# Kernel optimization log

Measured on AMD Instinct MI355X. Metric: run time of the kernel, lower is better.

Reference implementation:

```python
import jax, jax.numpy as jnp
import numpy as np

B, TE, TD, DE, DD = 4, 256, 256, 512, 512


def setup_inputs() -> dict:
    key = jax.random.key(0)
    k1, k2, k3, k4, k5 = jax.random.split(key, 5)
    return {
        "encoder_outputs": jax.random.normal(k1, (B, TE, DE), dtype=jnp.float32),
        "decoder_outputs": jax.random.normal(k2, (B, TD, DD), dtype=jnp.float32),
        "U_a": jax.random.normal(k3, (DE, DE), dtype=jnp.float32) * 0.05,
        "W_a": jax.random.normal(k4, (DD, DE), dtype=jnp.float32) * 0.05,
        "V_a": jax.random.normal(k5, (DE,), dtype=jnp.float32) * 0.05,
    }


def reference(encoder_outputs, decoder_outputs, U_a, W_a, V_a):
    # U_a_dot_h: [B, Te, De] -- precomputed once, as in the original
    Uh = jnp.einsum("bec,cd->bed", encoder_outputs, U_a)
    # W_a_dot_s for all decoder steps at once (original loops over t): [B, Td, De]
    Ws = jnp.einsum("btc,cd->btd", decoder_outputs, W_a)
    # additive energies: tanh(Uh + Ws) . V_a -> [B, Td, Te]
    e = jnp.einsum("bted,d->bte", jnp.tanh(Uh[:, None, :, :] + Ws[:, :, None, :]), V_a)
    attn = jax.nn.softmax(e, axis=-1)  # softmax over encoder timesteps
    # context: weighted sum of encoder outputs -> [B, Td, De]
    context = jnp.einsum("bte,bec->btc", attn, encoder_outputs)
    return context, attn
```

## Files before the change

### kernel.cpp

```cpp
#include <hip/hip_runtime.h>

#define B_    4
#define TE_   256
#define TD_   256
#define DE_   512
#define K_    512

typedef __attribute__((ext_vector_type(8))) short bf16x8;
typedef __attribute__((ext_vector_type(4))) float f32x4;

#define C1F 2.8853900817779268f

__device__ __forceinline__ ushort f2bf(float x) {
  uint u = __float_as_uint(x);
  return (ushort)((u + 0x7fffu + ((u >> 16) & 1u)) >> 16);
}
__device__ __forceinline__ float bf2f(ushort h) {
  return __uint_as_float(((uint)h) << 16);
}
__device__ __forceinline__ float exp2_fast(float x) {
  float r;
  asm("v_exp_f32 %0, %1" : "=v"(r) : "v"(x));
  return r;
}

__global__ __launch_bounds__(256) void conv_hilo(
    const float* __restrict__ enc, const float* __restrict__ dec,
    ushort* __restrict__ ehi, ushort* __restrict__ elo,
    ushort* __restrict__ dhi, ushort* __restrict__ dlo) {
  const float* in = blockIdx.y ? dec : enc;
  ushort* hi = blockIdx.y ? dhi : ehi;
  ushort* lo = blockIdx.y ? dlo : elo;
  int i = (blockIdx.x * 256 + threadIdx.x) * 4;
  float4 v = *(const float4*)&in[i];
  ushort4 h, l;
  h.x = f2bf(v.x); l.x = f2bf(v.x - bf2f(h.x));
  h.y = f2bf(v.y); l.y = f2bf(v.y - bf2f(h.y));
  h.z = f2bf(v.z); l.z = f2bf(v.z - bf2f(h.z));
  h.w = f2bf(v.w); l.w = f2bf(v.w - bf2f(h.w));
  *(ushort4*)&hi[i] = h;
  *(ushort4*)&lo[i] = l;
}

__global__ __launch_bounds__(256) void conv_bt(
    const float* __restrict__ Ua, const float* __restrict__ Wa,
    ushort* __restrict__ uhi, ushort* __restrict__ ulo,
    ushort* __restrict__ whi, ushort* __restrict__ wlo) {
  const float* in = blockIdx.z ? Wa : Ua;
  ushort* thi = blockIdx.z ? whi : uhi;
  ushort* tlo = blockIdx.z ? wlo : ulo;
  __shared__ float tile[64][65];
  int k0 = blockIdx.y * 64, n0 = blockIdx.x * 64;
  int tid = threadIdx.x;
#pragma unroll
  for (int i = 0; i < 16; ++i) {
    int idx = tid + i * 256;
    int r = idx >> 6, c = idx & 63;
    tile[r][c] = in[(size_t)(k0 + r) * 512 + n0 + c];
  }
  __syncthreads();
#pragma unroll
  for (int i = 0; i < 16; ++i) {
    int idx = tid + i * 256;
    int rn = idx >> 6, ck = idx & 63;
    float x = tile[ck][rn] * C1F;
    ushort h = f2bf(x);
    size_t o = (size_t)(n0 + rn) * 512 + k0 + ck;
    thi[o] = h;
    tlo[o] = f2bf(x - bf2f(h));
  }
}

__global__ __launch_bounds__(256, 4) void gemm_mfma(
    const ushort* __restrict__ ehi, const ushort* __restrict__ elo,
    const ushort* __restrict__ dhi, const ushort* __restrict__ dlo,
    const ushort* __restrict__ uhi, const ushort* __restrict__ ulo,
    const ushort* __restrict__ whi, const ushort* __restrict__ wlo,
    float* __restrict__ EuT, float* __restrict__ Ew) {
  const ushort *Ahi, *Alo, *Bhi, *Blo;
  int tid = threadIdx.x, lane = tid & 63;
  int ti = blockIdx.x * 4 + (tid >> 6);
  int bm, bn;
  if (blockIdx.z == 0) {
    Ahi = uhi; Alo = ulo; Bhi = ehi; Blo = elo;
    bm = (ti >> 5) * 16; bn = (ti & 31) * 32;
  } else {
    Ahi = dhi; Alo = dlo; Bhi = whi; Blo = wlo;
    bm = (ti >> 4) * 16; bn = (ti & 15) * 32;
  }
  int frow = lane & 15, fk = (lane >> 4) * 8;
  size_t ao = (size_t)(bm + frow) * K_ + fk;
  size_t bo = (size_t)(bn + frow) * K_ + fk;
  const ushort* pah = Ahi + ao;
  const ushort* pal = Alo + ao;
  const ushort* pbh0 = Bhi + bo; const ushort* pbh1 = pbh0 + 16 * K_;
  const ushort* pbl0 = Blo + bo; const ushort* pbl1 = pbl0 + 16 * K_;
  f32x4 acc0 = {}, acc1 = {};
#pragma unroll 4
  for (int k0 = 0; k0 < K_; k0 += 32) {
    bf16x8 ah = *(const bf16x8*)&pah[k0];
    bf16x8 al = *(const bf16x8*)&pal[k0];
    bf16x8 bh0 = *(const bf16x8*)&pbh0[k0];
    bf16x8 bl0 = *(const bf16x8*)&pbl0[k0];
    bf16x8 bh1 = *(const bf16x8*)&pbh1[k0];
    bf16x8 bl1 = *(const bf16x8*)&pbl1[k0];
    acc0 = __builtin_amdgcn_mfma_f32_16x16x32_bf16(ah, bh0, acc0, 0, 0, 0);
    acc1 = __builtin_amdgcn_mfma_f32_16x16x32_bf16(ah, bh1, acc1, 0, 0, 0);
    acc0 = __builtin_amdgcn_mfma_f32_16x16x32_bf16(ah, bl0, acc0, 0, 0, 0);
    acc1 = __builtin_amdgcn_mfma_f32_16x16x32_bf16(ah, bl1, acc1, 0, 0, 0);
    acc0 = __builtin_amdgcn_mfma_f32_16x16x32_bf16(al, bh0, acc0, 0, 0, 0);
    acc1 = __builtin_amdgcn_mfma_f32_16x16x32_bf16(al, bh1, acc1, 0, 0, 0);
  }
  int m0 = bm + (lane >> 4) * 4;
#pragma unroll
  for (int j = 0; j < 2; ++j) {
    const f32x4& acc = j ? acc1 : acc0;
    int n0 = bn + j * 16 + (lane & 15);
    if (blockIdx.z == 0) {
      float* cb = EuT + (size_t)(n0 >> 8) * 131072 + (size_t)m0 * 256 + (n0 & 255);
#pragma unroll
      for (int r = 0; r < 4; ++r) cb[(size_t)r * 256] = exp2_fast(acc[r]);
    } else {
      float* cb = Ew + (size_t)m0 * 512 + n0;
#pragma unroll
      for (int r = 0; r < 4; ++r) cb[(size_t)r * 512] = exp2_fast(acc[r]);
    }
  }
}

__global__ __launch_bounds__(1024, 8) void fused_attn(
    const float* __restrict__ enc, const float* __restrict__ EuT,
    const float* __restrict__ Ew, const float* __restrict__ Va,
    float* __restrict__ out_ctx, float* __restrict__ out_attn) {
  int bt = blockIdx.x;
  int b  = bt >> 7;
  int t0 = (bt & 127) * 2;
  __shared__ float ew0_s[520], ew1_s[520], mv_s[520];
  __shared__ float part[32][260];
  __shared__ float att2[TE_ * 2];
  __shared__ float ctxp[2][2][512];
  __shared__ float redm[2][4], reds[2][4];
  int tid = threadIdx.x, lane = tid & 63, w = tid >> 6;

  if (tid < 512) {
    const float* ewr = Ew + (size_t)(b * TD_ + t0) * DE_;
    int pd = tid + (tid >> 6);
    ew0_s[pd] = ewr[tid];
    ew1_s[pd] = ewr[DE_ + tid];
    mv_s[pd]  = -2.0f * Va[tid];
  }
  __syncthreads();

  const float* up = EuT + (size_t)b * 131072 + (size_t)w * 32 * 256 + lane * 4;
  float a0[4] = {}, a1[4] = {};
#pragma unroll 4
  for (int row = 0; row < 32; ++row) {
    float4 u4 = *(const float4*)&up[row * 256];
    int d = w * 32 + row, pd = d + (d >> 6);
    float e0 = ew0_s[pd], e1 = ew1_s[pd], mv = mv_s[pd];
#pragma unroll
    for (int j = 0; j < 4; ++j) {
      float u = j == 0 ? u4.x : j == 1 ? u4.y : j == 2 ? u4.z : u4.w;
      a0[j] = fmaf(mv, __builtin_amdgcn_rcpf(fmaf(u, e0, 1.0f)), a0[j]);
      a1[j] = fmaf(mv, __builtin_amdgcn_rcpf(fmaf(u, e1, 1.0f)), a1[j]);
    }
  }
  *(float4*)&part[w * 2 + 0][lane * 4] = make_float4(a0[0], a0[1], a0[2], a0[3]);
  *(float4*)&part[w * 2 + 1][lane * 4] = make_float4(a1[0], a1[1], a1[2], a1[3]);
  __syncthreads();

  int t = tid >> 8, col = tid & 255;
  float x = 0.f, p = 0.f, m, s;
  if (tid < 512) {
#pragma unroll
    for (int ww = 0; ww < 16; ++ww) x += part[ww * 2 + t][col];
    m = x;
#pragma unroll
    for (int off = 32; off; off >>= 1) m = fmaxf(m, __shfl_xor(m, off));
    if (lane == 0) redm[t][w & 3] = m;
  }
  __syncthreads();
  if (tid < 512) {
    m = fmaxf(fmaxf(redm[t][0], redm[t][1]), fmaxf(redm[t][2], redm[t][3]));
    p = __expf(x - m);
    s = p;
#pragma unroll
    for (int off = 32; off; off >>= 1) s += __shfl_xor(s, off);
    if (lane == 0) reds[t][w & 3] = s;
  }
  __syncthreads();
  if (tid < 512) {
    s = reds[t][0] + reds[t][1] + reds[t][2] + reds[t][3];
    float a = p * __builtin_amdgcn_rcpf(s);
    att2[col * 2 + t] = a;
    out_attn[(size_t)(b * TD_ + t0 + t) * TE_ + col] = a;
  }
  __syncthreads();

  int d = tid & 511, half = tid >> 9;
  const float* enc_b = enc + (size_t)b * TE_ * DE_ + (size_t)half * 128 * DE_;
  float c0 = 0.f, c1 = 0.f;
#pragma unroll 4
  for (int ee = 0; ee < 128; ++ee) {
    float2 av = *(const float2*)&att2[(half * 128 + ee) * 2];
    float xv = enc_b[(size_t)ee * DE_ + d];
    c0 = fmaf(av.x, xv, c0);
    c1 = fmaf(av.y, xv, c1);
  }
  ctxp[half][0][d] = c0;
  ctxp[half][1][d] = c1;
  __syncthreads();
  int tt = tid >> 9, dd = tid & 511;
  out_ctx[(size_t)(b * TD_ + t0 + tt) * DE_ + dd] =
      ctxp[0][tt][dd] + ctxp[1][tt][dd];
}

extern "C" void kernel_launch(void* const* d_in, const int* in_sizes, int n_in,
                              void* d_out, int out_size, void* d_ws, size_t ws_size,
                              hipStream_t stream) {
  const float* enc = (const float*)d_in[0];
  const float* dec = (const float*)d_in[1];
  const float* Ua  = (const float*)d_in[2];
  const float* Wa  = (const float*)d_in[3];
  const float* Va  = (const float*)d_in[4];

  float* out_ctx  = (float*)d_out;
  float* out_attn = out_ctx + (size_t)B_ * TD_ * DE_;

  char* wsp = (char*)d_ws;
  float* EuT = (float*)wsp;             wsp += (size_t)B_ * DE_ * TE_ * 4;
  float* Ewm = (float*)wsp;             wsp += (size_t)B_ * TD_ * DE_ * 4;
  ushort* ehi = (ushort*)wsp;           wsp += (size_t)B_ * TE_ * DE_ * 2;
  ushort* elo = (ushort*)wsp;           wsp += (size_t)B_ * TE_ * DE_ * 2;
  ushort* dhi = (ushort*)wsp;           wsp += (size_t)B_ * TD_ * DE_ * 2;
  ushort* dlo = (ushort*)wsp;           wsp += (size_t)B_ * TD_ * DE_ * 2;
  ushort* uhi = (ushort*)wsp;           wsp += (size_t)K_ * DE_ * 2;
  ushort* ulo = (ushort*)wsp;           wsp += (size_t)K_ * DE_ * 2;
  ushort* whi = (ushort*)wsp;           wsp += (size_t)K_ * DE_ * 2;
  ushort* wlo = (ushort*)wsp;           wsp += (size_t)K_ * DE_ * 2;

  conv_hilo<<<dim3(512, 2), 256, 0, stream>>>(enc, dec, ehi, elo, dhi, dlo);
  conv_bt<<<dim3(8, 8, 2), 256, 0, stream>>>(Ua, Wa, uhi, ulo, whi, wlo);
  gemm_mfma<<<dim3(256, 1, 2), 256, 0, stream>>>(
      ehi, elo, dhi, dlo, uhi, ulo, whi, wlo, EuT, Ewm);
  fused_attn<<<512, 1024, 0, stream>>>(enc, EuT, Ewm, Va, out_ctx, out_attn);
}
```

Baseline: 123.5 us.

## Fuse bf16 hi/lo split conversion into the MFMA GEMM kernel

Removes the two separate conversion kernels that split fp32 inputs and the transposed, scaled weights into bf16 hi/lo buffers. The GEMM now reads fp32 directly, reading weight columns with strided loads, and does the split and scaling in registers before each MFMA. This drops two launches and the intermediate workspace traffic. In exchange, each wave redoes the conversion for data other waves share, and the strided column reads of Ua/Wa coalesce poorly.

```diff
diff --git a/kernel.cpp b/kernel.cpp
--- a/kernel.cpp
+++ b/kernel.cpp
@@ -24,92 +24,73 @@
   return r;
 }
 
-__global__ __launch_bounds__(256) void conv_hilo(
+struct HL { bf16x8 h, l; };
+
+__device__ __forceinline__ HL mk_hl(const float* v) {
+  HL r;
+#pragma unroll
+  for (int j = 0; j < 8; ++j) {
+    ushort hh = f2bf(v[j]);
+    r.h[j] = (short)hh;
+    r.l[j] = (short)f2bf(v[j] - bf2f(hh));
+  }
+  return r;
+}
+__device__ __forceinline__ HL cvt_row(const float* p) {
+  float4 a = *(const float4*)p, b = *(const float4*)(p + 4);
+  float v[8] = {a.x, a.y, a.z, a.w, b.x, b.y, b.z, b.w};
+  return mk_hl(v);
+}
+__device__ __forceinline__ HL cvt_col(const float* p) {
+  float v[8];
+#pragma unroll
+  for (int j = 0; j < 8; ++j) v[j] = p[(size_t)j * 512] * C1F;
+  return mk_hl(v);
+}
+
+__global__ __launch_bounds__(256, 2) void gemm_conv(
     const float* __restrict__ enc, const float* __restrict__ dec,
-    ushort* __restrict__ ehi, ushort* __restrict__ elo,
-    ushort* __restrict__ dhi, ushort* __restrict__ dlo) {
-  const float* in = blockIdx.y ? dec : enc;
-  ushort* hi = blockIdx.y ? dhi : ehi;
-  ushort* lo = blockIdx.y ? dlo : elo;
-  int i = (blockIdx.x * 256 + threadIdx.x) * 4;
-  float4 v = *(const float4*)&in[i];
-  ushort4 h, l;
-  h.x = f2bf(v.x); l.x = f2bf(v.x - bf2f(h.x));
-  h.y = f2bf(v.y); l.y = f2bf(v.y - bf2f(h.y));
-  h.z = f2bf(v.z); l.z = f2bf(v.z - bf2f(h.z));
-  h.w = f2bf(v.w); l.w = f2bf(v.w - bf2f(h.w));
-  *(ushort4*)&hi[i] = h;
-  *(ushort4*)&lo[i] = l;
-}
-
-__global__ __launch_bounds__(256) void conv_bt(
     const float* __restrict__ Ua, const float* __restrict__ Wa,
-    ushort* __restrict__ uhi, ushort* __restrict__ ulo,
-    ushort* __restrict__ whi, ushort* __restrict__ wlo) {
-  const float* in = blockIdx.z ? Wa : Ua;
-  ushort* thi = blockIdx.z ? whi : uhi;
-  ushort* tlo = blockIdx.z ? wlo : ulo;
-  __shared__ float tile[64][65];
-  int k0 = blockIdx.y * 64, n0 = blockIdx.x * 64;
-  int tid = threadIdx.x;
-#pragma unroll
-  for (int i = 0; i < 16; ++i) {
-    int idx = tid + i * 256;
-    int r = idx >> 6, c = idx & 63;
-    tile[r][c] = in[(size_t)(k0 + r) * 512 + n0 + c];
-  }
-  __syncthreads();
-#pragma unroll
-  for (int i = 0; i < 16; ++i) {
-    int idx = tid + i * 256;
-    int rn = idx >> 6, ck = idx & 63;
-    float x = tile[ck][rn] * C1F;
-    ushort h = f2bf(x);
-    size_t o = (size_t)(n0 + rn) * 512 + k0 + ck;
-    thi[o] = h;
-    tlo[o] = f2bf(x - bf2f(h));
-  }
-}
-
-__global__ __launch_bounds__(256, 4) void gemm_mfma(
-    const ushort* __restrict__ ehi, const ushort* __restrict__ elo,
-    const ushort* __restrict__ dhi, const ushort* __restrict__ dlo,
-    const ushort* __restrict__ uhi, const ushort* __restrict__ ulo,
-    const ushort* __restrict__ whi, const ushort* __restrict__ wlo,
     float* __restrict__ EuT, float* __restrict__ Ew) {
-  const ushort *Ahi, *Alo, *Bhi, *Blo;
   int tid = threadIdx.x, lane = tid & 63;
   int ti = blockIdx.x * 4 + (tid >> 6);
+  int frow = lane & 15, fk = (lane >> 4) * 8;
+  f32x4 acc0 = {}, acc1 = {};
   int bm, bn;
   if (blockIdx.z == 0) {
-    Ahi = uhi; Alo = ulo; Bhi = ehi; Blo = elo;
     bm = (ti >> 5) * 16; bn = (ti & 31) * 32;
+    const float* pA  = Ua + (size_t)fk * 512 + bm + frow;
+    const float* pB0 = enc + (size_t)(bn + frow) * 512 + fk;
+    const float* pB1 = enc + (size_t)(bn + 16 + frow) * 512 + fk;
+#pragma unroll 2
+    for (int k0 = 0; k0 < K_; k0 += 32) {
+      HL A  = cvt_col(pA + (size_t)k0 * 512);
+      HL B0 = cvt_row(pB0 + k0);
+      HL B1 = cvt_row(pB1 + k0);
+      acc0 = __builtin_amdgcn_mfma_f32_16x16x32_bf16(A.h, B0.h, acc0, 0, 0, 0);
+      acc1 = __builtin_amdgcn_mfma_f32_16x16x32_bf16(A.h, B1.h, acc1, 0, 0, 0);
+      acc0 = __builtin_amdgcn_mfma_f32_16x16x32_bf16(A.h, B0.l, acc0, 0, 0, 0);
+      acc1 = __builtin_amdgcn_mfma_f32_16x16x32_bf16(A.h, B1.l, acc1, 0, 0, 0);
+      acc0 = __builtin_amdgcn_mfma_f32_16x16x32_bf16(A.l, B0.h, acc0, 0, 0, 0);
+      acc1 = __builtin_amdgcn_mfma_f32_16x16x32_bf16(A.l, B1.h, acc1, 0, 0, 0);
+    }
   } else {
-    Ahi = dhi; Alo = dlo; Bhi = whi; Blo = wlo;
     bm = (ti >> 4) * 16; bn = (ti & 15) * 32;
-  }
-  int frow = lane & 15, fk = (lane >> 4) * 8;
-  size_t ao = (size_t)(bm + frow) * K_ + fk;
-  size_t bo = (size_t)(bn + frow) * K_ + fk;
-  const ushort* pah = Ahi + ao;
-  const ushort* pal = Alo + ao;
-  const ushort* pbh0 = Bhi + bo; const ushort* pbh1 = pbh0 + 16 * K_;
-  const ushort* pbl0 = Blo + bo; const ushort* pbl1 = pbl0 + 16 * K_;
-  f32x4 acc0 = {}, acc1 = {};
-#pragma unroll 4
-  for (int k0 = 0; k0 < K_; k0 += 32) {
-    bf16x8 ah = *(const bf16x8*)&pah[k0];
-    bf16x8 al = *(const bf16x8*)&pal[k0];
-    bf16x8 bh0 = *(const bf16x8*)&pbh0[k0];
-    bf16x8 bl0 = *(const bf16x8*)&pbl0[k0];
-    bf16x8 bh1 = *(const bf16x8*)&pbh1[k0];
-    bf16x8 bl1 = *(const bf16x8*)&pbl1[k0];
-    acc0 = __builtin_amdgcn_mfma_f32_16x16x32_bf16(ah, bh0, acc0, 0, 0, 0);
-    acc1 = __builtin_amdgcn_mfma_f32_16x16x32_bf16(ah, bh1, acc1, 0, 0, 0);
-    acc0 = __builtin_amdgcn_mfma_f32_16x16x32_bf16(ah, bl0, acc0, 0, 0, 0);
-    acc1 = __builtin_amdgcn_mfma_f32_16x16x32_bf16(ah, bl1, acc1, 0, 0, 0);
-    acc0 = __builtin_amdgcn_mfma_f32_16x16x32_bf16(al, bh0, acc0, 0, 0, 0);
-    acc1 = __builtin_amdgcn_mfma_f32_16x16x32_bf16(al, bh1, acc1, 0, 0, 0);
+    const float* pA  = dec + (size_t)(bm + frow) * 512 + fk;
+    const float* pB0 = Wa + (size_t)fk * 512 + bn + frow;
+    const float* pB1 = Wa + (size_t)fk * 512 + bn + 16 + frow;
+#pragma unroll 2
+    for (int k0 = 0; k0 < K_; k0 += 32) {
+      HL A  = cvt_row(pA + k0);
+      HL B0 = cvt_col(pB0 + (size_t)k0 * 512);
+      HL B1 = cvt_col(pB1 + (size_t)k0 * 512);
+      acc0 = __builtin_amdgcn_mfma_f32_16x16x32_bf16(A.h, B0.h, acc0, 0, 0, 0);
+      acc1 = __builtin_amdgcn_mfma_f32_16x16x32_bf16(A.h, B1.h, acc1, 0, 0, 0);
+      acc0 = __builtin_amdgcn_mfma_f32_16x16x32_bf16(A.h, B0.l, acc0, 0, 0, 0);
+      acc1 = __builtin_amdgcn_mfma_f32_16x16x32_bf16(A.h, B1.l, acc1, 0, 0, 0);
+      acc0 = __builtin_amdgcn_mfma_f32_16x16x32_bf16(A.l, B0.h, acc0, 0, 0, 0);
+      acc1 = __builtin_amdgcn_mfma_f32_16x16x32_bf16(A.l, B1.h, acc1, 0, 0, 0);
+    }
   }
   int m0 = bm + (lane >> 4) * 4;
 #pragma unroll
@@ -230,18 +211,7 @@
   char* wsp = (char*)d_ws;
   float* EuT = (float*)wsp;             wsp += (size_t)B_ * DE_ * TE_ * 4;
   float* Ewm = (float*)wsp;             wsp += (size_t)B_ * TD_ * DE_ * 4;
-  ushort* ehi = (ushort*)wsp;           wsp += (size_t)B_ * TE_ * DE_ * 2;
-  ushort* elo = (ushort*)wsp;           wsp += (size_t)B_ * TE_ * DE_ * 2;
-  ushort* dhi = (ushort*)wsp;           wsp += (size_t)B_ * TD_ * DE_ * 2;
-  ushort* dlo = (ushort*)wsp;           wsp += (size_t)B_ * TD_ * DE_ * 2;
-  ushort* uhi = (ushort*)wsp;           wsp += (size_t)K_ * DE_ * 2;
-  ushort* ulo = (ushort*)wsp;           wsp += (size_t)K_ * DE_ * 2;
-  ushort* whi = (ushort*)wsp;           wsp += (size_t)K_ * DE_ * 2;
-  ushort* wlo = (ushort*)wsp;           wsp += (size_t)K_ * DE_ * 2;
-
-  conv_hilo<<<dim3(512, 2), 256, 0, stream>>>(enc, dec, ehi, elo, dhi, dlo);
-  conv_bt<<<dim3(8, 8, 2), 256, 0, stream>>>(Ua, Wa, uhi, ulo, whi, wlo);
-  gemm_mfma<<<dim3(256, 1, 2), 256, 0, stream>>>(
-      ehi, elo, dhi, dlo, uhi, ulo, whi, wlo, EuT, Ewm);
+
+  gemm_conv<<<dim3(256, 1, 2), 256, 0, stream>>>(enc, dec, Ua, Wa, EuT, Ewm);
   fused_attn<<<512, 1024, 0, stream>>>(enc, EuT, Ewm, Va, out_ctx, out_attn);
 }
```

New measurement: 112.9 us. 1.09x faster.
